# Optimization experiments

Hardware: AMD Instinct MI355X
Metric: run time of the kernel (lower is better)

The kernel has to match this reference:

```python
import jax, jax.numpy as jnp
import numpy as np

L, CH, S = 4096, 512, 64
SAMPLE_RATE = 4096.0


def setup_inputs() -> dict:
    key = jax.random.key(0)
    kx, ka, kc = jax.random.split(key, 3)
    x = jax.random.normal(kx, (L, CH), dtype=jnp.float32)
    # original init: lognegA = log(arange(1..S)) broadcast over channels; any real values work
    lognegA = jnp.broadcast_to(jnp.log(jnp.arange(1, S + 1, dtype=jnp.float32)), (CH, S)) \
        + 0.0 * jax.random.normal(ka, (CH, S), dtype=jnp.float32)
    B = jnp.ones((CH, S), dtype=jnp.float32)
    C = 0.01 * jax.random.normal(kc, (CH, S), dtype=jnp.float32)  # nn.initializers.normal() stddev=0.01
    return {"x": x, "lognegA": lognegA, "B": B, "C": C}


def reference(x, lognegA, B, C):
    length = x.shape[0]
    dt = 1.0 / SAMPLE_RATE
    A = -jnp.exp(lognegA)                         # [C, S], strictly negative
    Bd = (jnp.exp(A * dt) - 1.0) * B / A          # discretized B, [C, S]
    # Vandermonde-style kernel: Ak[l, c, s] = exp(l * A[c, s] * dt)
    Ak = jnp.exp(jnp.einsum('l,cs->lcs', jnp.arange(length, dtype=x.dtype), A * dt))
    K = jnp.einsum('cs,lcs->lc', C * Bd, Ak)      # [L, C] per-channel kernel
    # per-channel full causal convolution, truncated to length
    y = jax.vmap(jnp.convolve, in_axes=1, out_axes=1)(x, K)[:length]
    return y
```

## Files before the change

### kernel.cpp

```cpp
#include <hip/hip_runtime.h>


namespace {

constexpr int L_ = 4096;
constexpr int CH_ = 512;
constexpr int S_ = 64;
constexpr float DT = 1.0f / 4096.0f;
constexpr int SC = S_ * CH_;
constexpr int SG = 16;
constexpr int T_ = 64;
constexpr int NC_ = L_ / T_;
constexpr int GJ = 16;
constexpr int NJ = NC_ / GJ;

__device__ __forceinline__ void params16(const float* __restrict__ la,
                                         const float* __restrict__ Bg,
                                         const float* __restrict__ Cg,
                                         int c, int s0, float* r, float* w) {
  const float4* lap = reinterpret_cast<const float4*>(la + c * S_ + s0);
  if (w == nullptr) {
#pragma unroll
    for (int q = 0; q < 4; ++q) {
      const float4 v = lap[q];
      const float a[4] = {v.x, v.y, v.z, v.w};
#pragma unroll
      for (int t = 0; t < 4; ++t) {
        const float A = -expf(a[t]);
        r[q * 4 + t] = expf(A * DT);
      }
    }
  } else {
    const float4* bp = reinterpret_cast<const float4*>(Bg + c * S_ + s0);
    const float4* cp = reinterpret_cast<const float4*>(Cg + c * S_ + s0);
#pragma unroll
    for (int q = 0; q < 4; ++q) {
      const float4 v = lap[q], bb = bp[q], cc = cp[q];
      const float a[4] = {v.x, v.y, v.z, v.w};
      const float bv[4] = {bb.x, bb.y, bb.z, bb.w};
      const float cv[4] = {cc.x, cc.y, cc.z, cc.w};
#pragma unroll
      for (int t = 0; t < 4; ++t) {
        const float A = -expf(a[t]);
        const float rr = expf(A * DT);
        r[q * 4 + t] = rr;
        w[q * 4 + t] = cv[t] * ((rr - 1.0f) * bv[t] / A);
      }
    }
  }
}

template <int T>
__global__ __launch_bounds__(256) void k_local(const float* __restrict__ x,
                                               const float* __restrict__ la,
                                               float* __restrict__ carry) {
  const int lane = threadIdx.x & 63;
  const int g = threadIdx.x >> 6;
  const int k = blockIdx.x >> 3;
  const int c = ((blockIdx.x & 7) << 6) + lane;
  const int s0 = g * SG;

  float r[SG], h[SG];
  params16(la, nullptr, nullptr, c, s0, r, nullptr);
#pragma unroll
  for (int i = 0; i < SG; ++i) h[i] = 0.0f;

  const float* xp = x + (size_t)k * T * CH_ + c;
#pragma unroll 8
  for (int l = 0; l < T; ++l) {
    const float xv = xp[l * CH_];
#pragma unroll
    for (int i = 0; i < SG; ++i) h[i] = fmaf(r[i], h[i], xv);
  }

  float* cw = carry + (size_t)k * SC + s0 * CH_ + c;
#pragma unroll
  for (int i = 0; i < SG; ++i) cw[i * CH_] = h[i];
}

__global__ __launch_bounds__(256) void k_comb(const float* __restrict__ la,
                                              float* __restrict__ carry) {
  __shared__ float aggs[NJ][64];
  const int p = threadIdx.x & 63;
  const int j = threadIdx.x >> 6;
  const int pid = (blockIdx.x << 6) + p;
  const int s = pid >> 9;
  const int c = pid & (CH_ - 1);

  const float A = -expf(la[c * S_ + s]);
  const float rT = expf(A * (DT * (float)T_));
  float rTG = rT * rT;
  rTG *= rTG;
  rTG *= rTG;
  rTG *= rTG;

  float v[GJ];
#pragma unroll
  for (int m = 0; m < GJ; ++m) v[m] = carry[(size_t)(j * GJ + m) * SC + pid];

  float agg = 0.0f;
#pragma unroll
  for (int m = 0; m < GJ; ++m) agg = fmaf(rT, agg, v[m]);
  aggs[j][p] = agg;
  __syncthreads();

  float G = 0.0f;
  for (int j2 = 0; j2 < j; ++j2) G = fmaf(rTG, G, aggs[j2][p]);

  float st = G;
#pragma unroll
  for (int m = 0; m < GJ; ++m) {
    carry[(size_t)(j * GJ + m) * SC + pid] = st;
    st = fmaf(rT, st, v[m]);
  }
}

template <int T, bool USE_CARRY>
__global__ __launch_bounds__(256) void k_scan(const float* __restrict__ x,
                                              const float* __restrict__ la,
                                              const float* __restrict__ Bg,
                                              const float* __restrict__ Cg,
                                              const float* __restrict__ carry,
                                              float* __restrict__ y) {
  __shared__ float lds[4][8][64];

  const int lane = threadIdx.x & 63;
  const int g = threadIdx.x >> 6;
  const int k = blockIdx.x >> 3;
  const int cb = (blockIdx.x & 7) << 6;
  const int c = cb + lane;
  const int s0 = g * SG;

  float r[SG], w[SG], h[SG];
  params16(la, Bg, Cg, c, s0, r, w);

  if (USE_CARRY) {
    const float* crd = carry + (size_t)k * SC + s0 * CH_ + c;
#pragma unroll
    for (int i = 0; i < SG; ++i) h[i] = crd[i * CH_];
  } else {
#pragma unroll
    for (int i = 0; i < SG; ++i) h[i] = 0.0f;
  }

  const float* xp = x + (size_t)k * T * CH_ + c;
  float* yp = y + (size_t)k * T * CH_;

  for (int l = 0; l < T; l += 8) {
    float part[8];
#pragma unroll
    for (int jj = 0; jj < 8; ++jj) {
      const float xv = xp[(l + jj) * CH_];
      float a0 = 0, a1 = 0, a2 = 0, a3 = 0;
#pragma unroll
      for (int i = 0; i < SG; i += 4) {
        h[i]     = fmaf(r[i],     h[i],     xv);
        h[i + 1] = fmaf(r[i + 1], h[i + 1], xv);
        h[i + 2] = fmaf(r[i + 2], h[i + 2], xv);
        h[i + 3] = fmaf(r[i + 3], h[i + 3], xv);
        a0 = fmaf(w[i],     h[i],     a0);
        a1 = fmaf(w[i + 1], h[i + 1], a1);
        a2 = fmaf(w[i + 2], h[i + 2], a2);
        a3 = fmaf(w[i + 3], h[i + 3], a3);
      }
      part[jj] = (a0 + a1) + (a2 + a3);
    }

#pragma unroll
    for (int jj = 0; jj < 8; ++jj) lds[g][jj][lane] = part[jj];
    __syncthreads();

#pragma unroll
    for (int p = 0; p < 2; ++p) {
      const int idx = (int)threadIdx.x + p * 256;
      const int jj = idx >> 6;
      const int ln = idx & 63;
      const float vv = (lds[0][jj][ln] + lds[1][jj][ln]) +
                       (lds[2][jj][ln] + lds[3][jj][ln]);
      yp[(size_t)(l + jj) * CH_ + cb + ln] = vv;
    }
    __syncthreads();
  }
}

}

extern "C" void kernel_launch(void* const* d_in, const int* in_sizes, int n_in,
                              void* d_out, int out_size, void* d_ws, size_t ws_size,
                              hipStream_t stream) {
  const float* x = (const float*)d_in[0];
  const float* la = (const float*)d_in[1];
  const float* B = (const float*)d_in[2];
  const float* C = (const float*)d_in[3];
  float* y = (float*)d_out;
  float* carry = (float*)d_ws;

  const size_t need = (size_t)NC_ * SC * sizeof(float);
  if (ws_size >= need) {
    k_local<T_><<<NC_ * 8, 256, 0, stream>>>(x, la, carry);
    k_comb<<<SC / 64, 256, 0, stream>>>(la, carry);
    k_scan<T_, true><<<NC_ * 8, 256, 0, stream>>>(x, la, B, C, carry, y);
  } else {
    k_scan<L_, false><<<8, 256, 0, stream>>>(x, la, B, C, carry, y);
  }
}
```

Measured before the change: 92.91 us.

## Replace three-kernel chunked scan with two-kernel strip prefix plus inline carry combine

Chunk size drops to 32 and the separate carry-combine kernel is removed. A strip kernel writes running per-chunk prefix states within strips of 8 chunks. Each scan block then rebuilds its incoming state from the strip-end states of all earlier strips plus the previous chunk's prefix, using repeated-squaring powers of the decay. This saves one launch and one read/write pass over the carry buffer, but each scan block now does redundant serial loads across earlier strips, and the powers by repeated squaring may lose some precision.

After: 107.6 us. 15.8% more time.

```diff
diff --git a/kernel.cpp b/kernel.cpp
--- a/kernel.cpp
+++ b/kernel.cpp
@@ -9,10 +9,10 @@
 constexpr float DT = 1.0f / 4096.0f;
 constexpr int SC = S_ * CH_;
 constexpr int SG = 16;
-constexpr int T_ = 64;
+constexpr int T_ = 32;
 constexpr int NC_ = L_ / T_;
-constexpr int GJ = 16;
-constexpr int NJ = NC_ / GJ;
+constexpr int CPS = 8;
+constexpr int NS = NC_ / CPS;
 
 __device__ __forceinline__ void params16(const float* __restrict__ la,
                                          const float* __restrict__ Bg,
@@ -50,14 +50,14 @@
   }
 }
 
-template <int T>
-__global__ __launch_bounds__(256) void k_local(const float* __restrict__ x,
-                                               const float* __restrict__ la,
-                                               float* __restrict__ carry) {
+__global__ __launch_bounds__(256, 4)
+void k_strip(const float* __restrict__ x, const float* __restrict__ la,
+             float* __restrict__ P) {
   const int lane = threadIdx.x & 63;
   const int g = threadIdx.x >> 6;
-  const int k = blockIdx.x >> 3;
-  const int c = ((blockIdx.x & 7) << 6) + lane;
+  const int strip = blockIdx.x >> 3;
+  const int cb = (blockIdx.x & 7) << 6;
+  const int c = cb + lane;
   const int s0 = g * SG;
 
   float r[SG], h[SG];
@@ -65,63 +65,26 @@
 #pragma unroll
   for (int i = 0; i < SG; ++i) h[i] = 0.0f;
 
-  const float* xp = x + (size_t)k * T * CH_ + c;
+  const float* xp = x + (size_t)strip * CPS * T_ * CH_ + c;
+  float* pp = P + (size_t)strip * CPS * SC + s0 * CH_ + c;
+
+  for (int m = 0; m < CPS; ++m) {
 #pragma unroll 8
-  for (int l = 0; l < T; ++l) {
-    const float xv = xp[l * CH_];
-#pragma unroll
-    for (int i = 0; i < SG; ++i) h[i] = fmaf(r[i], h[i], xv);
-  }
-
-  float* cw = carry + (size_t)k * SC + s0 * CH_ + c;
-#pragma unroll
-  for (int i = 0; i < SG; ++i) cw[i * CH_] = h[i];
-}
-
-__global__ __launch_bounds__(256) void k_comb(const float* __restrict__ la,
-                                              float* __restrict__ carry) {
-  __shared__ float aggs[NJ][64];
-  const int p = threadIdx.x & 63;
-  const int j = threadIdx.x >> 6;
-  const int pid = (blockIdx.x << 6) + p;
-  const int s = pid >> 9;
-  const int c = pid & (CH_ - 1);
-
-  const float A = -expf(la[c * S_ + s]);
-  const float rT = expf(A * (DT * (float)T_));
-  float rTG = rT * rT;
-  rTG *= rTG;
-  rTG *= rTG;
-  rTG *= rTG;
-
-  float v[GJ];
-#pragma unroll
-  for (int m = 0; m < GJ; ++m) v[m] = carry[(size_t)(j * GJ + m) * SC + pid];
-
-  float agg = 0.0f;
-#pragma unroll
-  for (int m = 0; m < GJ; ++m) agg = fmaf(rT, agg, v[m]);
-  aggs[j][p] = agg;
-  __syncthreads();
-
-  float G = 0.0f;
-  for (int j2 = 0; j2 < j; ++j2) G = fmaf(rTG, G, aggs[j2][p]);
-
-  float st = G;
-#pragma unroll
-  for (int m = 0; m < GJ; ++m) {
-    carry[(size_t)(j * GJ + m) * SC + pid] = st;
-    st = fmaf(rT, st, v[m]);
-  }
-}
-
-template <int T, bool USE_CARRY>
-__global__ __launch_bounds__(256) void k_scan(const float* __restrict__ x,
-                                              const float* __restrict__ la,
-                                              const float* __restrict__ Bg,
-                                              const float* __restrict__ Cg,
-                                              const float* __restrict__ carry,
-                                              float* __restrict__ y) {
+    for (int l = 0; l < T_; ++l) {
+      const float xv = xp[(m * T_ + l) * CH_];
+#pragma unroll
+      for (int i = 0; i < SG; ++i) h[i] = fmaf(r[i], h[i], xv);
+    }
+    float* pm = pp + (size_t)m * SC;
+#pragma unroll
+    for (int i = 0; i < SG; ++i) pm[i * CH_] = h[i];
+  }
+}
+
+__global__ __launch_bounds__(256, 4)
+void k_scan2(const float* __restrict__ x, const float* __restrict__ la,
+             const float* __restrict__ Bg, const float* __restrict__ Cg,
+             const float* __restrict__ P, float* __restrict__ y) {
   __shared__ float lds[4][8][64];
 
   const int lane = threadIdx.x & 63;
@@ -130,23 +93,47 @@
   const int cb = (blockIdx.x & 7) << 6;
   const int c = cb + lane;
   const int s0 = g * SG;
+  const int gs = k >> 3;
+  const int m = k & 7;
 
   float r[SG], w[SG], h[SG];
   params16(la, Bg, Cg, c, s0, r, w);
 
-  if (USE_CARRY) {
-    const float* crd = carry + (size_t)k * SC + s0 * CH_ + c;
-#pragma unroll
-    for (int i = 0; i < SG; ++i) h[i] = crd[i * CH_];
+  float rT[SG], rT8[SG];
+#pragma unroll
+  for (int i = 0; i < SG; ++i) {
+    float t = r[i];
+    t *= t; t *= t; t *= t; t *= t; t *= t;
+    rT[i] = t;
+    t *= t; t *= t; t *= t;
+    rT8[i] = t;
+  }
+
+  float G[SG];
+#pragma unroll
+  for (int i = 0; i < SG; ++i) G[i] = 0.0f;
+  for (int gp = 0; gp < gs; ++gp) {
+    const float* ap = P + ((size_t)gp * CPS + (CPS - 1)) * SC + s0 * CH_ + c;
+#pragma unroll
+    for (int i = 0; i < SG; ++i) G[i] = fmaf(rT8[i], G[i], ap[i * CH_]);
+  }
+  for (int t2 = 0; t2 < m; ++t2) {
+#pragma unroll
+    for (int i = 0; i < SG; ++i) G[i] *= rT[i];
+  }
+  if (m == 0) {
+#pragma unroll
+    for (int i = 0; i < SG; ++i) h[i] = G[i];
   } else {
-#pragma unroll
-    for (int i = 0; i < SG; ++i) h[i] = 0.0f;
-  }
-
-  const float* xp = x + (size_t)k * T * CH_ + c;
-  float* yp = y + (size_t)k * T * CH_;
-
-  for (int l = 0; l < T; l += 8) {
+    const float* prev = P + (size_t)(k - 1) * SC + s0 * CH_ + c;
+#pragma unroll
+    for (int i = 0; i < SG; ++i) h[i] = G[i] + prev[i * CH_];
+  }
+
+  const float* xp = x + (size_t)k * T_ * CH_ + c;
+  float* yp = y + (size_t)k * T_ * CH_;
+
+  for (int l = 0; l < T_; l += 8) {
     float part[8];
 #pragma unroll
     for (int jj = 0; jj < 8; ++jj) {
@@ -169,7 +156,61 @@
 #pragma unroll
     for (int jj = 0; jj < 8; ++jj) lds[g][jj][lane] = part[jj];
     __syncthreads();
-
+#pragma unroll
+    for (int p = 0; p < 2; ++p) {
+      const int idx = (int)threadIdx.x + p * 256;
+      const int jj = idx >> 6;
+      const int ln = idx & 63;
+      const float vv = (lds[0][jj][ln] + lds[1][jj][ln]) +
+                       (lds[2][jj][ln] + lds[3][jj][ln]);
+      yp[(size_t)(l + jj) * CH_ + cb + ln] = vv;
+    }
+    __syncthreads();
+  }
+}
+
+__global__ __launch_bounds__(256) void k_scan_full(const float* __restrict__ x,
+                                                   const float* __restrict__ la,
+                                                   const float* __restrict__ Bg,
+                                                   const float* __restrict__ Cg,
+                                                   float* __restrict__ y) {
+  __shared__ float lds[4][8][64];
+  const int lane = threadIdx.x & 63;
+  const int g = threadIdx.x >> 6;
+  const int cb = (blockIdx.x & 7) << 6;
+  const int c = cb + lane;
+  const int s0 = g * SG;
+
+  float r[SG], w[SG], h[SG];
+  params16(la, Bg, Cg, c, s0, r, w);
+#pragma unroll
+  for (int i = 0; i < SG; ++i) h[i] = 0.0f;
+
+  const float* xp = x + c;
+  float* yp = y;
+
+  for (int l = 0; l < L_; l += 8) {
+    float part[8];
+#pragma unroll
+    for (int jj = 0; jj < 8; ++jj) {
+      const float xv = xp[(size_t)(l + jj) * CH_];
+      float a0 = 0, a1 = 0, a2 = 0, a3 = 0;
+#pragma unroll
+      for (int i = 0; i < SG; i += 4) {
+        h[i]     = fmaf(r[i],     h[i],     xv);
+        h[i + 1] = fmaf(r[i + 1], h[i + 1], xv);
+        h[i + 2] = fmaf(r[i + 2], h[i + 2], xv);
+        h[i + 3] = fmaf(r[i + 3], h[i + 3], xv);
+        a0 = fmaf(w[i],     h[i],     a0);
+        a1 = fmaf(w[i + 1], h[i + 1], a1);
+        a2 = fmaf(w[i + 2], h[i + 2], a2);
+        a3 = fmaf(w[i + 3], h[i + 3], a3);
+      }
+      part[jj] = (a0 + a1) + (a2 + a3);
+    }
+#pragma unroll
+    for (int jj = 0; jj < 8; ++jj) lds[g][jj][lane] = part[jj];
+    __syncthreads();
 #pragma unroll
     for (int p = 0; p < 2; ++p) {
       const int idx = (int)threadIdx.x + p * 256;
@@ -193,14 +234,13 @@
   const float* B = (const float*)d_in[2];
   const float* C = (const float*)d_in[3];
   float* y = (float*)d_out;
-  float* carry = (float*)d_ws;
+  float* P = (float*)d_ws;
 
   const size_t need = (size_t)NC_ * SC * sizeof(float);
   if (ws_size >= need) {
-    k_local<T_><<<NC_ * 8, 256, 0, stream>>>(x, la, carry);
-    k_comb<<<SC / 64, 256, 0, stream>>>(la, carry);
-    k_scan<T_, true><<<NC_ * 8, 256, 0, stream>>>(x, la, B, C, carry, y);
+    k_strip<<<NS * 8, 256, 0, stream>>>(x, la, P);
+    k_scan2<<<NC_ * 8, 256, 0, stream>>>(x, la, B, C, P, y);
   } else {
-    k_scan<L_, false><<<8, 256, 0, stream>>>(x, la, B, C, carry, y);
-  }
-}
+    k_scan_full<<<8, 256, 0, stream>>>(x, la, B, C, y);
+  }
+}
```
